# Kernel tuning notes

Hardware: AMD Instinct MI355X
Metric: run time of the kernel (lower is better)

Reference implementation:

```python
import jax, jax.numpy as jnp
import numpy as np

T = 32.0                       # softmax temperature
THRESH = float(np.cos(np.pi * 40.0 / 180.0))  # cos(degree), degree=40
NEG_INF = -9.0e15


def setup_inputs() -> dict:
    key = jax.random.key(0)
    ks = jax.random.split(key, 11)
    B, C, D_IMG, D_ATT, H_ATT, H = 2048, 1000, 2048, 312, 128, 128
    def rn(k, shape, scale=1.0):
        return jax.random.normal(k, shape, dtype=jnp.float32) * scale
    return {
        "image_feats": rn(ks[0], (B, D_IMG)),
        "img_proto":   rn(ks[1], (C, D_IMG)),
        "attributes":  rn(ks[2], (C, D_ATT)),
        "unused":      0,
        # parameters
        "att_g":   rn(ks[3], (D_ATT, H_ATT), 0.05),
        "slim_w":  rn(ks[4], (D_IMG, D_ATT), 0.02),   # proto_slim weight (transposed torch layout)
        "slim_b":  rn(ks[5], (D_ATT,), 0.02),
        "img_w":   rn(ks[6], (D_IMG, H), 0.02),
        "proto_w": rn(ks[7], (2 * D_ATT, H), 0.02),   # att_dim + proto_red_dim = 624
        "proto_b": rn(ks[8], (1, H), 0.02),
        "fc_w":    rn(ks[9], (H, 1), 0.05),
        "fc_b":    rn(ks[10], (1,), 0.05),
    }


def reference(image_feats, img_proto, attributes, unused,
              att_g, slim_w, slim_b, img_w, proto_w, proto_b, fc_w, fc_b):
    # proto_slim: [C, D_img] -> [C, att_dim]
    proto_red = img_proto @ slim_w + slim_b

    # --- get_attention: cosine similarity among attribute projections ---
    g = attributes @ att_g                                   # [C, att_hC] (g == h in original)
    gn = g / jnp.clip(jnp.linalg.norm(g, axis=1, keepdims=True), 1e-12)
    sim = gn @ gn.T                                          # [C, C] cosine similarity
    raw = jnp.where(sim > THRESH, sim, NEG_INF)              # threshold mask
    attn = jax.nn.softmax(raw * T, axis=1)                   # [C, C]

    # --- propagate prototypes ---
    att_outs = attn @ attributes                             # [C, att_dim]
    img_proto_outs = attn @ proto_red                        # [C, att_dim]
    outs = jnp.concatenate([att_outs, img_proto_outs], axis=1)  # [C, 2*att_dim]

    # --- relation MLP (broadcast instead of materialized expand+matmul) ---
    img_h = image_feats @ img_w                              # [B, H]
    proto_h = outs @ proto_w                                 # [C, H]
    hidden = jax.nn.relu(img_h[:, None, :] + proto_h[None, :, :] + proto_b)  # [B, C, H]
    outputs = hidden @ fc_w + fc_b                           # [B, C, 1]
    return outputs[..., 0]                                   # [B, C]
```

## Files before the change

kernel.cpp:

```cpp
#include <hip/hip_runtime.h>

typedef unsigned short ushort_t;
typedef __bf16 bf16x8 __attribute__((ext_vector_type(8)));
typedef float f32x4 __attribute__((ext_vector_type(4)));
typedef float f32x2 __attribute__((ext_vector_type(2)));
typedef ushort_t us4 __attribute__((ext_vector_type(4)));

#define T_SOFT 32.0f
#define THRESH 0.76604444311897803f
#define SW 1048
#define SO 648

__device__ __forceinline__ ushort_t f2bf(float f) {
  union { float f; unsigned u; } x; x.f = f;
  unsigned r = (x.u + 0x7fffu + ((x.u >> 16) & 1u)) >> 16;
  return (ushort_t)r;
}
__device__ __forceinline__ float bf2f(ushort_t h) {
  union { unsigned u; float f; } x; x.u = ((unsigned)h) << 16; return x.f;
}

__device__ __forceinline__ us4 pack4(float4 x) {
  union { unsigned u[2]; us4 h; } r;
  union { float4 f; unsigned u[4]; } a;
  a.f = x;
  r.u[0] = __builtin_amdgcn_perm(a.u[1] + 0x8000u, a.u[0] + 0x8000u, 0x07060302u);
  r.u[1] = __builtin_amdgcn_perm(a.u[3] + 0x8000u, a.u[2] + 0x8000u, 0x07060302u);
  return r.h;
}
__device__ __forceinline__ bf16x8 pack8(float4 x, float4 y) {
  union { unsigned u[4]; bf16x8 h; } r;
  union { float4 f; unsigned u[4]; } a, b;
  a.f = x; b.f = y;
  r.u[0] = __builtin_amdgcn_perm(a.u[1] + 0x8000u, a.u[0] + 0x8000u, 0x07060302u);
  r.u[1] = __builtin_amdgcn_perm(a.u[3] + 0x8000u, a.u[2] + 0x8000u, 0x07060302u);
  r.u[2] = __builtin_amdgcn_perm(b.u[1] + 0x8000u, b.u[0] + 0x8000u, 0x07060302u);
  r.u[3] = __builtin_amdgcn_perm(b.u[3] + 0x8000u, b.u[2] + 0x8000u, 0x07060302u);
  return r.h;
}

__global__ __launch_bounds__(256) void tr3_k(const float* __restrict__ s0, ushort_t* __restrict__ d0,
                                             const float* __restrict__ s1, ushort_t* __restrict__ d1,
                                             const float* __restrict__ s2, ushort_t* __restrict__ d2,
                                             const float* __restrict__ s3, ushort_t* __restrict__ d3,
                                             ushort_t* __restrict__ gn_bf,
                                             float* __restrict__ z0, float* __restrict__ z1) {
  int b = blockIdx.x, tid = threadIdx.x;
  if (b >= 1296) {
    if (b == 1296) {
      us4 z = {0, 0, 0, 0};
      *reinterpret_cast<us4*>(gn_bf + 1000 * 128 + tid * 4) = z;
    } else if (b < 1361) {
      int local = b - 1297;
      float4 z = make_float4(0.f, 0.f, 0.f, 0.f);
      float4* p = reinterpret_cast<float4*>(z0) + local * 1024 + tid;
      p[0] = z; p[256] = z; p[512] = z; p[768] = z;
    } else {
      int local = b - 1361;
      float4 z = make_float4(0.f, 0.f, 0.f, 0.f);
      float4* p = reinterpret_cast<float4*>(z1) + local * 1024 + tid;
      p[0] = z; p[256] = z; p[512] = z; p[768] = z;
    }
    return;
  }
  __shared__ float tl[32][33];
  const float* src; ushort_t* dst; int R, C, Cw, Rpad, local, ctiles;
  if (b < 640)       { src = s0; dst = d0; R = 2048; C = 312; Cw = 320; Rpad = 2048; local = b;       ctiles = 10; }
  else if (b < 896)  { src = s1; dst = d1; R = 2048; C = 128; Cw = 128; Rpad = 2048; local = b - 640; ctiles = 4;  }
  else if (b < 976)  { src = s2; dst = d2; R = 624;  C = 128; Cw = 128; Rpad = 640;  local = b - 896; ctiles = 4;  }
  else               { src = s3; dst = d3; R = 1000; C = 312; Cw = 312; Rpad = 1024; local = b - 976; ctiles = 10; }
  int rt = local / ctiles, ct = local - rt * ctiles;
  int r0 = rt * 32, c0 = ct * 32;
  #pragma unroll
  for (int p = 0; p < 4; ++p) {
    int idx = p * 256 + tid;
    int rr = idx >> 5, cc = idx & 31;
    float v = 0.f;
    if (r0 + rr < R && c0 + cc < C) v = src[(size_t)(r0 + rr) * C + (c0 + cc)];
    tl[cc][rr] = v;
  }
  __syncthreads();
  int cc = tid >> 3, rq = tid & 7;
  if (c0 + cc < Cw) {
    us4 o;
    o[0] = f2bf(tl[cc][rq * 4 + 0]);
    o[1] = f2bf(tl[cc][rq * 4 + 1]);
    o[2] = f2bf(tl[cc][rq * 4 + 2]);
    o[3] = f2bf(tl[cc][rq * 4 + 3]);
    *reinterpret_cast<us4*>(dst + (size_t)(c0 + cc) * Rpad + r0 + rq * 4) = o;
  }
}

__device__ __forceinline__ void gemm_f32a_seg(
    const float* __restrict__ A, int M, int lda,
    const ushort_t* __restrict__ BT, int ldbt,
    float* __restrict__ C, int ldc,
    int r0, int k0, int nsteps,
    ushort_t* __restrict__ As, ushort_t* __restrict__ Bs, int tid) {
  const int SA = 72;
  int lane = tid & 63, wv = tid >> 6;
  int l15 = lane & 15, quad = lane >> 4;
  int arow = tid >> 4, akq = tid & 15;
  int brow = tid >> 3, bkq = tid & 7;
  const float* agp[8];
  #pragma unroll
  for (int p = 0; p < 8; ++p) {
    int r = r0 + arow + p * 16; if (r >= M) r = M - 1;
    agp[p] = A + (size_t)r * lda + k0 + akq * 4;
  }
  const ushort_t* bgp[4];
  #pragma unroll
  for (int p = 0; p < 4; ++p) bgp[p] = BT + (size_t)(brow + p * 32) * ldbt + k0 + bkq * 8;

  float4 ap[8]; bf16x8 bp[4];
  #pragma unroll
  for (int p = 0; p < 8; ++p) ap[p] = *reinterpret_cast<const float4*>(agp[p]);
  #pragma unroll
  for (int p = 0; p < 4; ++p) bp[p] = *reinterpret_cast<const bf16x8*>(bgp[p]);

  f32x4 acc[2][8];
  #pragma unroll
  for (int i = 0; i < 2; ++i)
    #pragma unroll
    for (int j = 0; j < 8; ++j) acc[i][j] = f32x4{0.f, 0.f, 0.f, 0.f};

  for (int s = 0; s < nsteps; ++s) {
    if (s) __syncthreads();
    #pragma unroll
    for (int p = 0; p < 8; ++p)
      *reinterpret_cast<us4*>(As + (arow + p * 16) * SA + akq * 4) = pack4(ap[p]);
    #pragma unroll
    for (int p = 0; p < 4; ++p)
      *reinterpret_cast<bf16x8*>(Bs + (brow + p * 32) * SA + bkq * 8) = bp[p];
    if (s + 1 < nsteps) {
      #pragma unroll
      for (int p = 0; p < 8; ++p) ap[p] = *reinterpret_cast<const float4*>(agp[p] + 64);
      #pragma unroll
      for (int p = 0; p < 4; ++p) bp[p] = *reinterpret_cast<const bf16x8*>(bgp[p] + 64);
      #pragma unroll
      for (int p = 0; p < 8; ++p) agp[p] += 64;
      #pragma unroll
      for (int p = 0; p < 4; ++p) bgp[p] += 64;
    }
    __syncthreads();
    #pragma unroll
    for (int kh = 0; kh < 2; ++kh) {
      bf16x8 af[2];
      #pragma unroll
      for (int pi = 0; pi < 2; ++pi)
        af[pi] = *reinterpret_cast<bf16x8*>(As + ((wv * 2 + pi) * 16 + l15) * SA + kh * 32 + quad * 8);
      #pragma unroll
      for (int ct = 0; ct < 8; ++ct) {
        bf16x8 bfr = *reinterpret_cast<bf16x8*>(Bs + (ct * 16 + l15) * SA + kh * 32 + quad * 8);
        acc[0][ct] = __builtin_amdgcn_mfma_f32_16x16x32_bf16(af[0], bfr, acc[0][ct], 0, 0, 0);
        acc[1][ct] = __builtin_amdgcn_mfma_f32_16x16x32_bf16(af[1], bfr, acc[1][ct], 0, 0, 0);
      }
    }
  }
  #pragma unroll
  for (int pi = 0; pi < 2; ++pi)
    #pragma unroll
    for (int ct = 0; ct < 8; ++ct) {
      int col = ct * 16 + l15;
      #pragma unroll
      for (int r = 0; r < 4; ++r) {
        int row = r0 + (wv * 2 + pi) * 16 + quad * 4 + r;
        if (row < M) atomicAdd(&C[(size_t)row * ldc + col], acc[pi][ct][r]);
      }
    }
}

__device__ __forceinline__ void gemm_protoT_seg(
    const ushort_t* __restrict__ A, const float* __restrict__ B,
    float* __restrict__ outp, int r0, int c0, int k0, int nsteps,
    ushort_t* __restrict__ As, ushort_t* __restrict__ Bs, int tid) {
  const int SA = 72;
  int lane = tid & 63, wv = tid >> 6;
  int l15 = lane & 15, quad = lane >> 4;
  int frow = tid >> 4, fkq = tid & 15;
  int hrow = tid >> 3, hkq = tid & 7;
  const ushort_t* agp[4];
  #pragma unroll
  for (int p = 0; p < 4; ++p) {
    int r = r0 + hrow + p * 32; if (r >= 320) r = 319;
    agp[p] = A + (size_t)r * 2048 + k0 + hkq * 8;
  }
  const float* bgp[8];
  #pragma unroll
  for (int p = 0; p < 8; ++p) {
    int n = c0 + frow + p * 16; if (n >= 1000) n = 999;
    bgp[p] = B + (size_t)n * 2048 + k0 + fkq * 4;
  }
  bf16x8 ar[4]; float4 br[8];
  #pragma unroll
  for (int p = 0; p < 4; ++p) ar[p] = *reinterpret_cast<const bf16x8*>(agp[p]);
  #pragma unroll
  for (int p = 0; p < 8; ++p) br[p] = *reinterpret_cast<const float4*>(bgp[p]);

  f32x4 acc[2][8];
  #pragma unroll
  for (int i = 0; i < 2; ++i)
    #pragma unroll
    for (int j = 0; j < 8; ++j) acc[i][j] = f32x4{0.f, 0.f, 0.f, 0.f};

  for (int s = 0; s < nsteps; ++s) {
    if (s) __syncthreads();
    #pragma unroll
    for (int p = 0; p < 4; ++p)
      *reinterpret_cast<bf16x8*>(As + (hrow + p * 32) * SA + hkq * 8) = ar[p];
    #pragma unroll
    for (int p = 0; p < 8; ++p)
      *reinterpret_cast<us4*>(Bs + (frow + p * 16) * SA + fkq * 4) = pack4(br[p]);
    if (s + 1 < nsteps) {
      #pragma unroll
      for (int p = 0; p < 4; ++p) ar[p] = *reinterpret_cast<const bf16x8*>(agp[p] + 64);
      #pragma unroll
      for (int p = 0; p < 8; ++p) br[p] = *reinterpret_cast<const float4*>(bgp[p] + 64);
      #pragma unroll
      for (int p = 0; p < 4; ++p) agp[p] += 64;
      #pragma unroll
      for (int p = 0; p < 8; ++p) bgp[p] += 64;
    }
    __syncthreads();
    #pragma unroll
    for (int kh = 0; kh < 2; ++kh) {
      bf16x8 af[2];
      #pragma unroll
      for (int pi = 0; pi < 2; ++pi)
        af[pi] = *reinterpret_cast<bf16x8*>(As + ((wv * 2 + pi) * 16 + l15) * SA + kh * 32 + quad * 8);
      #pragma unroll
      for (int ct = 0; ct < 8; ++ct) {
        bf16x8 bfr = *reinterpret_cast<bf16x8*>(Bs + (ct * 16 + l15) * SA + kh * 32 + quad * 8);
        acc[0][ct] = __builtin_amdgcn_mfma_f32_16x16x32_bf16(af[0], bfr, acc[0][ct], 0, 0, 0);
        acc[1][ct] = __builtin_amdgcn_mfma_f32_16x16x32_bf16(af[1], bfr, acc[1][ct], 0, 0, 0);
      }
    }
  }
  #pragma unroll
  for (int pi = 0; pi < 2; ++pi)
    #pragma unroll
    for (int ct = 0; ct < 8; ++ct) {
      int n = c0 + ct * 16 + l15;
      if (n < 1000) {
        #pragma unroll
        for (int r = 0; r < 4; ++r) {
          int m = r0 + (wv * 2 + pi) * 16 + quad * 4 + r;
          if (m < 320) atomicAdd(&outp[(size_t)m * 1024 + n], acc[pi][ct][r]);
        }
      }
    }
}

__global__ __launch_bounds__(256, 4) void mega_k(
    const float* __restrict__ attributes, const float* __restrict__ att_g,
    ushort_t* __restrict__ gn_bf,
    const float* __restrict__ img_proto, const ushort_t* __restrict__ slimT,
    const float* __restrict__ image_feats, const ushort_t* __restrict__ imgwT,
    float* __restrict__ img_h, float* __restrict__ proto_redT) {
  __shared__ ushort_t As[128 * 72];
  __shared__ ushort_t Bs[128 * 72];
  int b = blockIdx.x, tid = threadIdx.x;
  if (b < 128) {
    int tile = b >> 3, kc = b & 7;
    gemm_f32a_seg(image_feats, 2048, 2048, imgwT, 2048, img_h, 128,
                  tile * 128, kc * 256, 4, As, Bs, tid);
    return;
  }
  if (b < 320) {
    int idx = b - 128;
    int tile = idx >> 3, kc = idx & 7;
    int rb = tile / 8, cb = tile - rb * 8;
    gemm_protoT_seg(slimT, img_proto, proto_redT, rb * 128, cb * 128, kc * 256, 4, As, Bs, tid);
    return;
  }
  b -= 320;
  float* a_lds = reinterpret_cast<float*>(As);
  float* red2 = reinterpret_cast<float*>(Bs);
  int h = tid & 127;
  int c0 = b * 8;
  for (int idx = tid; idx < 8 * 312; idx += 256) {
    int r = idx / 312;
    int k = idx - r * 312;
    a_lds[r * 316 + k] = attributes[(c0 + r) * 312 + k];
  }
  __syncthreads();
  float acc[8] = {0.f,0.f,0.f,0.f,0.f,0.f,0.f,0.f};
  for (int k = 0; k < 312; k += 4) {
    float w0 = att_g[(k + 0) * 128 + h];
    float w1 = att_g[(k + 1) * 128 + h];
    float w2 = att_g[(k + 2) * 128 + h];
    float w3 = att_g[(k + 3) * 128 + h];
    #pragma unroll
    for (int r = 0; r < 8; ++r) {
      float4 a4 = *reinterpret_cast<const float4*>(&a_lds[r * 316 + k]);
      acc[r] += a4.x * w0 + a4.y * w1 + a4.z * w2 + a4.w * w3;
    }
  }
  int lane = tid & 63, wvid = (tid >> 6) & 1;
  #pragma unroll
  for (int r = 0; r < 8; ++r) {
    float v = acc[r] * acc[r];
    #pragma unroll
    for (int off = 32; off > 0; off >>= 1) v += __shfl_xor(v, off, 64);
    if (lane == 0) red2[r * 2 + wvid] = v;
  }
  __syncthreads();
  #pragma unroll
  for (int r = 0; r < 8; ++r) {
    float nrm = fmaxf(sqrtf(red2[r * 2 + 0] + red2[r * 2 + 1]), 1e-12f);
    gn_bf[(c0 + r) * 128 + h] = f2bf(acc[r] / nrm);
  }
}

__global__ __launch_bounds__(256) void attn4_k(
    const ushort_t* __restrict__ gn_bf, const ushort_t* __restrict__ attrT,
    const float* __restrict__ proto_redT,
    const float* __restrict__ slim_b, const ushort_t* __restrict__ protowT,
    const float* __restrict__ proto_b, float* __restrict__ ph) {
  __shared__ ushort_t W[16 * SW];
  __shared__ ushort_t OS[16 * SO];
  __shared__ float rsum[16];
  __shared__ int flags[63];
  int tid = threadIdx.x;
  int i0 = blockIdx.x * 16;
  int lane = tid & 63, wv = tid >> 6;
  int l15 = lane & 15, quad = lane >> 4;
  if (tid < 63) flags[tid] = 0;
  if (tid >= 64 && tid < 80) rsum[tid - 64] = 0.f;
  W[(tid >> 4) * SW + 1008 + (tid & 15)] = 0;
  __syncthreads();

  const ushort_t* abase = gn_bf + (size_t)(i0 + l15) * 128 + quad * 8;
  bf16x8 af0 = *reinterpret_cast<const bf16x8*>(abase);
  bf16x8 af1 = *reinterpret_cast<const bf16x8*>(abase + 32);
  bf16x8 af2 = *reinterpret_cast<const bf16x8*>(abase + 64);
  bf16x8 af3 = *reinterpret_cast<const bf16x8*>(abase + 96);
  float rs[4] = {0.f, 0.f, 0.f, 0.f};
  for (int jt = wv; jt < 63; jt += 4) {
    const ushort_t* bbase = gn_bf + (size_t)(jt * 16 + l15) * 128 + quad * 8;
    f32x4 d = {0.f, 0.f, 0.f, 0.f};
    d = __builtin_amdgcn_mfma_f32_16x16x32_bf16(af0, *reinterpret_cast<const bf16x8*>(bbase),      d, 0, 0, 0);
    d = __builtin_amdgcn_mfma_f32_16x16x32_bf16(af1, *reinterpret_cast<const bf16x8*>(bbase + 32), d, 0, 0, 0);
    d = __builtin_amdgcn_mfma_f32_16x16x32_bf16(af2, *reinterpret_cast<const bf16x8*>(bbase + 64), d, 0, 0, 0);
    d = __builtin_amdgcn_mfma_f32_16x16x32_bf16(af3, *reinterpret_cast<const bf16x8*>(bbase + 96), d, 0, 0, 0);
    int hot = 0;
    #pragma unroll
    for (int r = 0; r < 4; ++r) {
      float w = 0.f;
      if (d[r] > THRESH) { w = __expf(T_SOFT * (d[r] - 1.0f)); hot = 1; }
      ushort_t wb = f2bf(w);
      W[(quad * 4 + r) * SW + jt * 16 + l15] = wb;
      rs[r] += bf2f(wb);
    }
    if (hot) flags[jt] = 1;
  }
  #pragma unroll
  for (int r = 0; r < 4; ++r) {
    float v = rs[r];
    v += __shfl_xor(v, 1, 64); v += __shfl_xor(v, 2, 64);
    v += __shfl_xor(v, 4, 64); v += __shfl_xor(v, 8, 64);
    if (l15 == 0) atomicAdd(&rsum[quad * 4 + r], v);
  }
  __syncthreads();

  f32x4 acc[10];
  #pragma unroll
  for (int t = 0; t < 10; ++t) acc[t] = f32x4{0.f, 0.f, 0.f, 0.f};
  for (int s = 0; s < 32; ++s) {
    int f = flags[2 * s] | ((2 * s + 1 < 63) ? flags[2 * s + 1] : 0);
    if (!f) continue;
    bf16x8 a = *reinterpret_cast<bf16x8*>(W + l15 * SW + s * 32 + quad * 8);
    #pragma unroll
    for (int t = 0; t < 10; ++t) {
      int nrow = (wv * 10 + t) * 16 + l15;
      bf16x8 bfr;
      if (nrow < 312) {
        bfr = *reinterpret_cast<const bf16x8*>(attrT + (size_t)nrow * 1024 + s * 32 + quad * 8);
      } else if (nrow < 632) {
        const float* pp = proto_redT + (size_t)(nrow - 312) * 1024 + s * 32 + quad * 8;
        bfr = pack8(*reinterpret_cast<const float4*>(pp), *reinterpret_cast<const float4*>(pp + 4));
      } else {
        union { unsigned u[4]; bf16x8 h; } z = {{0u, 0u, 0u, 0u}};
        bfr = z.h;
      }
      acc[t] = __builtin_amdgcn_mfma_f32_16x16x32_bf16(a, bfr, acc[t], 0, 0, 0);
    }
  }
  #pragma unroll
  for (int t = 0; t < 10; ++t) {
    int col = (wv * 10 + t) * 16 + l15;
    float bias = (col >= 312 && col < 624) ? slim_b[col - 312] : 0.f;
    #pragma unroll
    for (int r = 0; r < 4; ++r) {
      int row = quad * 4 + r;
      float inv = 1.f / fmaxf(rsum[row], 1e-30f);
      OS[row * SO + col] = f2bf(acc[t][r] * inv + bias);
    }
  }
  __syncthreads();

  f32x4 acc2[2];
  acc2[0] = f32x4{0.f, 0.f, 0.f, 0.f};
  acc2[1] = f32x4{0.f, 0.f, 0.f, 0.f};
  for (int s = 0; s < 20; ++s) {
    bf16x8 a = *reinterpret_cast<bf16x8*>(OS + l15 * SO + s * 32 + quad * 8);
    #pragma unroll
    for (int t = 0; t < 2; ++t) {
      int n = (wv * 2 + t) * 16 + l15;
      bf16x8 bfr = *reinterpret_cast<const bf16x8*>(protowT + (size_t)n * 640 + s * 32 + quad * 8);
      acc2[t] = __builtin_amdgcn_mfma_f32_16x16x32_bf16(a, bfr, acc2[t], 0, 0, 0);
    }
  }
  #pragma unroll
  for (int t = 0; t < 2; ++t) {
    int h = (wv * 2 + t) * 16 + l15;
    float pb = proto_b[h];
    #pragma unroll
    for (int r = 0; r < 4; ++r) {
      int gi = i0 + quad * 4 + r;
      if (gi < 1000) ph[(size_t)gi * 128 + h] = acc2[t][r] + pb;
    }
  }
}

__global__ __launch_bounds__(256) void final_k(
    const float* __restrict__ img_h, const float* __restrict__ ph,
    const float* __restrict__ fc_w, const float* __restrict__ fc_b,
    float* __restrict__ out) {
  __shared__ float ih[128][132];
  __shared__ float ps[64][132];
  __shared__ float ws_[128];
  int tid = threadIdx.x;
  int b0 = blockIdx.x * 128;
  int c0 = blockIdx.y * 64;
  for (int idx = tid; idx < 4096; idx += 256) {
    int row = idx >> 5, c4 = (idx & 31) * 4;
    float4 v = *reinterpret_cast<const float4*>(img_h + (size_t)(b0 + row) * 128 + c4);
    *reinterpret_cast<float4*>(&ih[row][c4]) = v;
  }
  for (int idx = tid; idx < 2048; idx += 256) {
    int row = idx >> 5, c4 = (idx & 31) * 4;
    int c = c0 + row;
    float4 v = make_float4(0.f, 0.f, 0.f, 0.f);
    if (c < 1000) v = *reinterpret_cast<const float4*>(ph + (size_t)c * 128 + c4);
    *reinterpret_cast<float4*>(&ps[row][c4]) = v;
  }
  if (tid < 128) ws_[tid] = fc_w[tid];
  __syncthreads();
  int tx = tid & 15, ty = tid >> 4;
  f32x2 acc[8][4] = {};
  const f32x2 zero2 = {0.f, 0.f};
  for (int h = 0; h < 128; h += 4) {
    float4 w4 = *reinterpret_cast<float4*>(&ws_[h]);
    f32x2 wlo = {w4.x, w4.y}, whi = {w4.z, w4.w};
    float4 a4[8], p4[4];
    #pragma unroll
    for (int i = 0; i < 8; ++i) a4[i] = *reinterpret_cast<float4*>(&ih[ty * 8 + i][h]);
    #pragma unroll
    for (int j = 0; j < 4; ++j) p4[j] = *reinterpret_cast<float4*>(&ps[tx * 4 + j][h]);
    #pragma unroll
    for (int i = 0; i < 8; ++i) {
      f32x2 alo = {a4[i].x, a4[i].y}, ahi = {a4[i].z, a4[i].w};
      #pragma unroll
      for (int j = 0; j < 4; ++j) {
        f32x2 plo = {p4[j].x, p4[j].y}, phi = {p4[j].z, p4[j].w};
        f32x2 t0 = __builtin_elementwise_max(alo + plo, zero2);
        f32x2 t1 = __builtin_elementwise_max(ahi + phi, zero2);
        acc[i][j] = acc[i][j] + t0 * wlo;
        acc[i][j] = acc[i][j] + t1 * whi;
      }
    }
  }
  float fb = fc_b[0];
  #pragma unroll
  for (int i = 0; i < 8; ++i) {
    int b = b0 + ty * 8 + i;
    int c = c0 + tx * 4;
    if (c < 1000) {
      float4 v = make_float4(acc[i][0].x + acc[i][0].y + fb, acc[i][1].x + acc[i][1].y + fb,
                             acc[i][2].x + acc[i][2].y + fb, acc[i][3].x + acc[i][3].y + fb);
      *reinterpret_cast<float4*>(out + (size_t)b * 1000 + c) = v;
    }
  }
}

extern "C" void kernel_launch(void* const* d_in, const int* in_sizes, int n_in,
                              void* d_out, int out_size, void* d_ws, size_t ws_size,
                              hipStream_t stream) {
  const float* image_feats = (const float*)d_in[0];
  const float* img_proto   = (const float*)d_in[1];
  const float* attributes  = (const float*)d_in[2];
  const float* att_g   = (const float*)d_in[4];
  const float* slim_w  = (const float*)d_in[5];
  const float* slim_b  = (const float*)d_in[6];
  const float* img_w   = (const float*)d_in[7];
  const float* proto_w = (const float*)d_in[8];
  const float* proto_b = (const float*)d_in[9];
  const float* fc_w    = (const float*)d_in[10];
  const float* fc_b    = (const float*)d_in[11];
  float* out = (float*)d_out;

  char* ws = (char*)d_ws;
  size_t o = 0;
  auto alloc = [&](size_t bytes) { size_t r = o; o += (bytes + 255) & ~(size_t)255; return r; };
  ushort_t* imgwT   = (ushort_t*)(ws + alloc(128ull * 2048 * 2));
  ushort_t* slimT   = (ushort_t*)(ws + alloc(320ull * 2048 * 2));
  ushort_t* protowT = (ushort_t*)(ws + alloc(128ull * 640 * 2));
  ushort_t* gn_bf   = (ushort_t*)(ws + alloc(1008ull * 128 * 2));
  ushort_t* attrT   = (ushort_t*)(ws + alloc(312ull * 1024 * 2));
  float* proto_redT = (float*)(ws + alloc(320ull * 1024 * 4));
  float* img_h     = (float*)(ws + alloc(2048ull * 128 * 4));
  float* ph        = (float*)(ws + alloc(1000ull * 128 * 4));

  tr3_k<<<1441, 256, 0, stream>>>(slim_w, slimT, img_w, imgwT, proto_w, protowT,
                                  attributes, attrT, gn_bf, img_h, proto_redT);

  mega_k<<<445, 256, 0, stream>>>(attributes, att_g, gn_bf,
                                  img_proto, slimT,
                                  image_feats, imgwT, img_h, proto_redT);

  attn4_k<<<63, 256, 0, stream>>>(gn_bf, attrT, proto_redT, slim_b, protowT, proto_b, ph);

  final_k<<<dim3(16, 16), 256, 0, stream>>>(img_h, ph, fc_w, fc_b, out);
}
```

Measured before the change: 182.6 us.

## Replace split-K atomics with partial buffers reduced by consumer kernels

The split-K GEMMs for img_h and proto_red now write per-K-chunk partial results to separate buffers with plain stores, replacing atomicAdd into zero-initialised outputs. The split factor drops from 8 to 4, giving each block twice as many K steps and reducing the grid from 445 to 285 blocks. The consumers (attn4_k and final_k) sum the four partials on load, and the zeroing blocks are removed from the transpose kernel. This removes atomic traffic and the zero-fill, but increases workspace, adds extra reads in the consumers, and lowers parallelism in the GEMM phase. The launch-bounds occupancy hint on mega_k is also dropped.

```diff
diff --git a/kernel.cpp b/kernel.cpp
--- a/kernel.cpp
+++ b/kernel.cpp
@@ -10,6 +10,8 @@
 #define THRESH 0.76604444311897803f
 #define SW 1048
 #define SO 648
+#define PIH (2048 * 128)
+#define PPR (320 * 1024)
 
 __device__ __forceinline__ ushort_t f2bf(float f) {
   union { float f; unsigned u; } x; x.f = f;
@@ -28,9 +30,9 @@
   r.u[1] = __builtin_amdgcn_perm(a.u[3] + 0x8000u, a.u[2] + 0x8000u, 0x07060302u);
   return r.h;
 }
-__device__ __forceinline__ bf16x8 pack8(float4 x, float4 y) {
+__device__ __forceinline__ bf16x8 pack8(f32x4 x, f32x4 y) {
   union { unsigned u[4]; bf16x8 h; } r;
-  union { float4 f; unsigned u[4]; } a, b;
+  union { f32x4 f; unsigned u[4]; } a, b;
   a.f = x; b.f = y;
   r.u[0] = __builtin_amdgcn_perm(a.u[1] + 0x8000u, a.u[0] + 0x8000u, 0x07060302u);
   r.u[1] = __builtin_amdgcn_perm(a.u[3] + 0x8000u, a.u[2] + 0x8000u, 0x07060302u);
@@ -43,24 +45,11 @@
                                              const float* __restrict__ s1, ushort_t* __restrict__ d1,
                                              const float* __restrict__ s2, ushort_t* __restrict__ d2,
                                              const float* __restrict__ s3, ushort_t* __restrict__ d3,
-                                             ushort_t* __restrict__ gn_bf,
-                                             float* __restrict__ z0, float* __restrict__ z1) {
+                                             ushort_t* __restrict__ gn_bf) {
   int b = blockIdx.x, tid = threadIdx.x;
   if (b >= 1296) {
-    if (b == 1296) {
-      us4 z = {0, 0, 0, 0};
-      *reinterpret_cast<us4*>(gn_bf + 1000 * 128 + tid * 4) = z;
-    } else if (b < 1361) {
-      int local = b - 1297;
-      float4 z = make_float4(0.f, 0.f, 0.f, 0.f);
-      float4* p = reinterpret_cast<float4*>(z0) + local * 1024 + tid;
-      p[0] = z; p[256] = z; p[512] = z; p[768] = z;
-    } else {
-      int local = b - 1361;
-      float4 z = make_float4(0.f, 0.f, 0.f, 0.f);
-      float4* p = reinterpret_cast<float4*>(z1) + local * 1024 + tid;
-      p[0] = z; p[256] = z; p[512] = z; p[768] = z;
-    }
+    us4 z = {0, 0, 0, 0};
+    *reinterpret_cast<us4*>(gn_bf + 1000 * 128 + tid * 4) = z;
     return;
   }
   __shared__ float tl[32][33];
@@ -92,9 +81,9 @@
 }
 
 __device__ __forceinline__ void gemm_f32a_seg(
-    const float* __restrict__ A, int M, int lda,
+    const float* __restrict__ A, int lda,
     const ushort_t* __restrict__ BT, int ldbt,
-    float* __restrict__ C, int ldc,
+    float* __restrict__ Cpart, int ldc,
     int r0, int k0, int nsteps,
     ushort_t* __restrict__ As, ushort_t* __restrict__ Bs, int tid) {
   const int SA = 72;
@@ -104,10 +93,7 @@
   int brow = tid >> 3, bkq = tid & 7;
   const float* agp[8];
   #pragma unroll
-  for (int p = 0; p < 8; ++p) {
-    int r = r0 + arow + p * 16; if (r >= M) r = M - 1;
-    agp[p] = A + (size_t)r * lda + k0 + akq * 4;
-  }
+  for (int p = 0; p < 8; ++p) agp[p] = A + (size_t)(r0 + arow + p * 16) * lda + k0 + akq * 4;
   const ushort_t* bgp[4];
   #pragma unroll
   for (int p = 0; p < 4; ++p) bgp[p] = BT + (size_t)(brow + p * 32) * ldbt + k0 + bkq * 8;
@@ -165,7 +151,7 @@
       #pragma unroll
       for (int r = 0; r < 4; ++r) {
         int row = r0 + (wv * 2 + pi) * 16 + quad * 4 + r;
-        if (row < M) atomicAdd(&C[(size_t)row * ldc + col], acc[pi][ct][r]);
+        Cpart[(size_t)row * ldc + col] = acc[pi][ct][r];
       }
     }
 }
@@ -241,39 +227,38 @@
     #pragma unroll
     for (int ct = 0; ct < 8; ++ct) {
       int n = c0 + ct * 16 + l15;
-      if (n < 1000) {
-        #pragma unroll
-        for (int r = 0; r < 4; ++r) {
-          int m = r0 + (wv * 2 + pi) * 16 + quad * 4 + r;
-          if (m < 320) atomicAdd(&outp[(size_t)m * 1024 + n], acc[pi][ct][r]);
-        }
+      #pragma unroll
+      for (int r = 0; r < 4; ++r) {
+        int m = r0 + (wv * 2 + pi) * 16 + quad * 4 + r;
+        if (m < 320) outp[(size_t)m * 1024 + n] = acc[pi][ct][r];
       }
     }
 }
 
-__global__ __launch_bounds__(256, 4) void mega_k(
+__global__ __launch_bounds__(256) void mega_k(
     const float* __restrict__ attributes, const float* __restrict__ att_g,
     ushort_t* __restrict__ gn_bf,
     const float* __restrict__ img_proto, const ushort_t* __restrict__ slimT,
     const float* __restrict__ image_feats, const ushort_t* __restrict__ imgwT,
-    float* __restrict__ img_h, float* __restrict__ proto_redT) {
+    float* __restrict__ img_hP, float* __restrict__ proto_redP) {
   __shared__ ushort_t As[128 * 72];
   __shared__ ushort_t Bs[128 * 72];
   int b = blockIdx.x, tid = threadIdx.x;
-  if (b < 128) {
-    int tile = b >> 3, kc = b & 7;
-    gemm_f32a_seg(image_feats, 2048, 2048, imgwT, 2048, img_h, 128,
-                  tile * 128, kc * 256, 4, As, Bs, tid);
+  if (b < 64) {
+    int tile = b >> 2, kc = b & 3;
+    gemm_f32a_seg(image_feats, 2048, imgwT, 2048, img_hP + (size_t)kc * PIH, 128,
+                  tile * 128, kc * 512, 8, As, Bs, tid);
     return;
   }
-  if (b < 320) {
-    int idx = b - 128;
-    int tile = idx >> 3, kc = idx & 7;
-    int rb = tile / 8, cb = tile - rb * 8;
-    gemm_protoT_seg(slimT, img_proto, proto_redT, rb * 128, cb * 128, kc * 256, 4, As, Bs, tid);
+  if (b < 160) {
+    int idx = b - 64;
+    int tile = idx >> 2, kc = idx & 3;
+    int rb = tile >> 3, cb = tile & 7;
+    gemm_protoT_seg(slimT, img_proto, proto_redP + (size_t)kc * PPR,
+                    rb * 128, cb * 128, kc * 512, 8, As, Bs, tid);
     return;
   }
-  b -= 320;
+  b -= 160;
   float* a_lds = reinterpret_cast<float*>(As);
   float* red2 = reinterpret_cast<float*>(Bs);
   int h = tid & 127;
@@ -314,7 +299,7 @@
 
 __global__ __launch_bounds__(256) void attn4_k(
     const ushort_t* __restrict__ gn_bf, const ushort_t* __restrict__ attrT,
-    const float* __restrict__ proto_redT,
+    const float* __restrict__ proto_redP,
     const float* __restrict__ slim_b, const ushort_t* __restrict__ protowT,
     const float* __restrict__ proto_b, float* __restrict__ ph) {
   __shared__ ushort_t W[16 * SW];
@@ -377,8 +362,12 @@
       if (nrow < 312) {
         bfr = *reinterpret_cast<const bf16x8*>(attrT + (size_t)nrow * 1024 + s * 32 + quad * 8);
       } else if (nrow < 632) {
-        const float* pp = proto_redT + (size_t)(nrow - 312) * 1024 + s * 32 + quad * 8;
-        bfr = pack8(*reinterpret_cast<const float4*>(pp), *reinterpret_cast<const float4*>(pp + 4));
+        const float* pp = proto_redP + (size_t)(nrow - 312) * 1024 + s * 32 + quad * 8;
+        f32x4 x = *reinterpret_cast<const f32x4*>(pp)       + *reinterpret_cast<const f32x4*>(pp + PPR)
+                + *reinterpret_cast<const f32x4*>(pp + 2 * PPR) + *reinterpret_cast<const f32x4*>(pp + 3 * PPR);
+        f32x4 y = *reinterpret_cast<const f32x4*>(pp + 4)   + *reinterpret_cast<const f32x4*>(pp + PPR + 4)
+                + *reinterpret_cast<const f32x4*>(pp + 2 * PPR + 4) + *reinterpret_cast<const f32x4*>(pp + 3 * PPR + 4);
+        bfr = pack8(x, y);
       } else {
         union { unsigned u[4]; bf16x8 h; } z = {{0u, 0u, 0u, 0u}};
         bfr = z.h;
@@ -424,7 +413,7 @@
 }
 
 __global__ __launch_bounds__(256) void final_k(
-    const float* __restrict__ img_h, const float* __restrict__ ph,
+    const float* __restrict__ img_hP, const float* __restrict__ ph,
     const float* __restrict__ fc_w, const float* __restrict__ fc_b,
     float* __restrict__ out) {
   __shared__ float ih[128][132];
@@ -435,8 +424,10 @@
   int c0 = blockIdx.y * 64;
   for (int idx = tid; idx < 4096; idx += 256) {
     int row = idx >> 5, c4 = (idx & 31) * 4;
-    float4 v = *reinterpret_cast<const float4*>(img_h + (size_t)(b0 + row) * 128 + c4);
-    *reinterpret_cast<float4*>(&ih[row][c4]) = v;
+    const float* p = img_hP + (size_t)(b0 + row) * 128 + c4;
+    f32x4 v = *reinterpret_cast<const f32x4*>(p)           + *reinterpret_cast<const f32x4*>(p + PIH)
+            + *reinterpret_cast<const f32x4*>(p + 2 * PIH) + *reinterpret_cast<const f32x4*>(p + 3 * PIH);
+    *reinterpret_cast<f32x4*>(&ih[row][c4]) = v;
   }
   for (int idx = tid; idx < 2048; idx += 256) {
     int row = idx >> 5, c4 = (idx & 31) * 4;
@@ -508,18 +499,18 @@
   ushort_t* protowT = (ushort_t*)(ws + alloc(128ull * 640 * 2));
   ushort_t* gn_bf   = (ushort_t*)(ws + alloc(1008ull * 128 * 2));
   ushort_t* attrT   = (ushort_t*)(ws + alloc(312ull * 1024 * 2));
-  float* proto_redT = (float*)(ws + alloc(320ull * 1024 * 4));
-  float* img_h     = (float*)(ws + alloc(2048ull * 128 * 4));
+  float* proto_redP = (float*)(ws + alloc(4ull * PPR * 4));
+  float* img_hP    = (float*)(ws + alloc(4ull * PIH * 4));
   float* ph        = (float*)(ws + alloc(1000ull * 128 * 4));
 
-  tr3_k<<<1441, 256, 0, stream>>>(slim_w, slimT, img_w, imgwT, proto_w, protowT,
-                                  attributes, attrT, gn_bf, img_h, proto_redT);
-
-  mega_k<<<445, 256, 0, stream>>>(attributes, att_g, gn_bf,
+  tr3_k<<<1297, 256, 0, stream>>>(slim_w, slimT, img_w, imgwT, proto_w, protowT,
+                                  attributes, attrT, gn_bf);
+
+  mega_k<<<285, 256, 0, stream>>>(attributes, att_g, gn_bf,
                                   img_proto, slimT,
-                                  image_feats, imgwT, img_h, proto_redT);
-
-  attn4_k<<<63, 256, 0, stream>>>(gn_bf, attrT, proto_redT, slim_b, protowT, proto_b, ph);
-
-  final_k<<<dim3(16, 16), 256, 0, stream>>>(img_h, ph, fc_w, fc_b, out);
-}
+                                  image_feats, imgwT, img_hP, proto_redP);
+
+  attn4_k<<<63, 256, 0, stream>>>(gn_bf, attrT, proto_redP, slim_b, protowT, proto_b, ph);
+
+  final_k<<<dim3(16, 16), 256, 0, stream>>>(img_hP, ph, fc_w, fc_b, out);
+}
```

Result: faster. 176.4 us (-3.4%).
